# Kernel tuning notes

Measured on AMD Instinct MI355X. Metric: run time of the kernel, lower is better.

Reference implementation:

```python
import jax, jax.numpy as jnp
import numpy as np

N_RAYS = 16384
NS = 128
FD = 32
HID = 64
GS = 128
NEAR = 0.1
FAR = 100.0  # unused by the original forward body
EARLY_TERM = 1e-4


def mip360_contract(c):
    # inf-norm scene contraction (Mip-NeRF 360); safe denom avoids NaN grads in untaken branch
    norm = jnp.max(jnp.abs(c), axis=-1, keepdims=True)
    ns = jnp.maximum(norm, 1.0)
    return jnp.where(norm <= 1.0, c, (2.0 - 1.0 / ns) * c / ns) / 2.0


def grid_sample_trilinear(grid, coords):
    # torch.nn.functional.grid_sample 5D, mode='bilinear', padding='zeros', align_corners=False
    # grid: [D,H,W]; coords[...,0]=x->W, coords[...,1]=y->H, coords[...,2]=z->D, in [-1,1]
    D, H, W = grid.shape
    x = ((coords[..., 0] + 1.0) * W - 1.0) * 0.5
    y = ((coords[..., 1] + 1.0) * H - 1.0) * 0.5
    z = ((coords[..., 2] + 1.0) * D - 1.0) * 0.5
    x0 = jnp.floor(x); y0 = jnp.floor(y); z0 = jnp.floor(z)
    fx = x - x0; fy = y - y0; fz = z - z0
    x0 = x0.astype(jnp.int32); y0 = y0.astype(jnp.int32); z0 = z0.astype(jnp.int32)

    def corner(zi, yi, xi):
        valid = ((zi >= 0) & (zi < D) & (yi >= 0) & (yi < H) & (xi >= 0) & (xi < W))
        v = grid[jnp.clip(zi, 0, D - 1), jnp.clip(yi, 0, H - 1), jnp.clip(xi, 0, W - 1)]
        return v * valid.astype(grid.dtype)

    out = (corner(z0, y0, x0) * (1 - fz) * (1 - fy) * (1 - fx)
           + corner(z0, y0, x0 + 1) * (1 - fz) * (1 - fy) * fx
           + corner(z0, y0 + 1, x0) * (1 - fz) * fy * (1 - fx)
           + corner(z0, y0 + 1, x0 + 1) * (1 - fz) * fy * fx
           + corner(z0 + 1, y0, x0) * fz * (1 - fy) * (1 - fx)
           + corner(z0 + 1, y0, x0 + 1) * fz * (1 - fy) * fx
           + corner(z0 + 1, y0 + 1, x0) * fz * fy * (1 - fx)
           + corner(z0 + 1, y0 + 1, x0 + 1) * fz * fy * fx)
    return out


def setup_inputs() -> dict:
    key = jax.random.key(0)
    ks = jax.random.split(key, 9)
    rays_o = jax.random.normal(ks[0], (N_RAYS, 3), jnp.float32) * 0.1
    rd = jax.random.normal(ks[1], (N_RAYS, 3), jnp.float32)
    rays_d = rd / jnp.linalg.norm(rd, axis=-1, keepdims=True)
    grid = (jax.random.uniform(ks[2], (GS, GS, GS)) > 0.3).astype(jnp.float32)

    def lin(k, fin, fout):
        return jax.random.normal(k, (fin, fout), jnp.float32) * (1.0 / np.sqrt(fin))

    return {
        "rays_o": rays_o, "rays_d": rays_d, "grid": grid,
        "W1": lin(ks[3], 3, HID), "b1": jnp.zeros(HID, jnp.float32),
        "W2": lin(ks[4], HID, FD), "b2": jnp.zeros(FD, jnp.float32),
        "Ws": lin(ks[5], FD, 1), "bs": jnp.zeros(1, jnp.float32),
        "Wr1": lin(ks[6], FD + 3, HID), "br1": jnp.zeros(HID, jnp.float32),
        "Wr2": lin(ks[7], HID, 3), "br2": jnp.zeros(3, jnp.float32),
        "n_samples": NS,
    }


def reference(rays_o, rays_d, grid, W1, b1, W2, b2, Ws, bs, Wr1, br1, Wr2, br2, n_samples):
    n = rays_o.shape[0]
    half = n_samples // 2
    t_close = jnp.linspace(NEAR, NEAR + 1.0, half, dtype=jnp.float32)
    t_far = jnp.exp(jnp.arange(half, dtype=jnp.float32) * np.float32(np.log(1.0 + 1.0 / 256.0))) * (NEAR + 1.0)
    t_values = jnp.concatenate([t_close, t_far])
    distances = t_values[1:] - t_values[:-1]          # [S]
    t_values = t_values[:-1]                          # [S], S = n_samples - 1 (eval mode: no jitter)

    samples = rays_o[:, None, :] + rays_d[:, None, :] * t_values[None, :, None]   # [n,S,3]
    sc = mip360_contract(samples)
    occ = grid_sample_trilinear(grid, sc)             # [n,S]
    mask = occ > 0.0                                  # .bool() of sampled occupancy
    maskf = mask.astype(sc.dtype)

    # feature MLP; zero where unmasked (torch scatters into a zeros buffer)
    feat = jax.nn.relu(sc @ W1 + b1) @ W2 + b2        # [n,S,FD]
    feat = feat * maskf[..., None]
    sigma = jax.nn.softplus(feat @ Ws + bs)[..., 0] * maskf   # [n,S]

    alpha_log = -sigma * distances[None, :]
    trans = jnp.exp(jnp.cumsum(alpha_log, axis=1))
    trans = jnp.concatenate([jnp.ones((n, 1), sc.dtype), trans[:, :-1]], axis=1)
    alpha = 1.0 - jnp.exp(alpha_log)
    weights = trans * alpha                           # [n,S]

    mask2 = mask & (weights > EARLY_TERM)
    dirs = jnp.broadcast_to(rays_d[:, None, :], samples.shape)
    h = jax.nn.relu(jnp.concatenate([feat, dirs], axis=-1) @ Wr1 + br1)
    rgb = jax.nn.sigmoid(h @ Wr2 + br2) * weights[..., None]
    rgb = rgb * mask2[..., None].astype(sc.dtype)
    return rgb.sum(axis=1)                            # [n,3]
```

## Files before the change

### kernel.cpp

```cpp
#include <hip/hip_runtime.h>
#include <math.h>

#define HID 64
#define FD 32
#define ROWB 144

typedef __fp16 f16x8 __attribute__((ext_vector_type(8)));
typedef float  f32x4 __attribute__((ext_vector_type(4)));
typedef unsigned int u32x4 __attribute__((ext_vector_type(4)));
typedef unsigned int u32x2 __attribute__((ext_vector_type(2)));

__device__ __forceinline__ unsigned int pk2(float a, float b) {
    auto v = __builtin_amdgcn_cvt_pkrtz(a, b);
    return __builtin_bit_cast(unsigned int, v);
}
__device__ __forceinline__ f32x4 mfma16(f16x8 a, f16x8 b, f32x4 c) {
    return __builtin_amdgcn_mfma_f32_16x16x32_f16(a, b, c, 0, 0, 0);
}

__global__ void prep(const float* __restrict__ W2,  const float* __restrict__ Ws,
                     const float* __restrict__ bs,  const float* __restrict__ b2,
                     const float* __restrict__ Wr1, const float* __restrict__ Wr2,
                     unsigned char* __restrict__ wsb) {
    __shared__ float wv[64];
    const int t = threadIdx.x;
    if (t < 64) {
        float acc = 0.f;
        for (int k = 0; k < FD; ++k) acc = fmaf(W2[t*FD+k], Ws[k], acc);
        wv[t] = acc;
    }
    __syncthreads();
    if (t < 48) {
        float v = 0.f;
        if (t < 32) v = b2[t];
        else if (t == 32) {
            float c = bs[0];
            for (int k = 0; k < FD; ++k) c = fmaf(b2[k], Ws[k], c);
            v = c;
        }
        ((float*)(wsb + 16384))[t] = v;
    }
    const int f = t >> 6, lane = t & 63;
    const int c15 = lane & 15, g = lane >> 4;
    f16x8 o;
    #pragma unroll
    for (int j = 0; j < 8; ++j) {
        float v = 0.f;
        if (f < 6) {
            int mt = f >> 1, kc = f & 1, row = 16*mt + c15;
            int kg = 32*kc + 8*g + j;
            v = (row < 32) ? W2[kg*FD + row] : ((row == 32) ? wv[kg] : 0.f);
        } else if (f < 14) {
            int ff = f - 6, mt = ff >> 1, kc = ff & 1, row = 16*mt + c15;
            int kg = 32*kc + 8*g + j;
            v = (kg < FD+3) ? Wr1[kg*HID + row] : 0.f;
        } else {
            int kc = f - 14, row = c15;
            int kg = 32*kc + 8*g + j;
            v = (row < 3) ? Wr2[kg*3 + row] : 0.f;
        }
        o[j] = (__fp16)v;
    }
    *(f16x8*)(wsb + (f*64 + lane)*16) = o;
}

__device__ __forceinline__ float t_of(int i) {
    #pragma clang fp contract(off)
    if (i < 64) {
        if (i == 63) return 1.1f;
        return (float)(0.1 + (double)i * (1.0 / 63.0));
    }
    const float LOGC = 0.0038986404159402954f;
    float arg = (float)(i - 64) * LOGC;
    return (float)exp((double)arg) * 1.1f;
}

__device__ __forceinline__ bool gv(const float* __restrict__ g, int zi, int yi, int xi) {
    bool ok = ((unsigned)zi < 128u) & ((unsigned)yi < 128u) & ((unsigned)xi < 128u);
    int zc = min(max(zi, 0), 127);
    int yc = min(max(yi, 0), 127);
    int xc = min(max(xi, 0), 127);
    float v = g[(((zc << 7) + yc) << 7) + xc];
    return ok & (v > 0.5f);
}

__global__ __launch_bounds__(256) void nerf_render(
    const float* __restrict__ rays_o, const float* __restrict__ rays_d,
    const float* __restrict__ grid,
    const float* __restrict__ W1,  const float* __restrict__ b1,
    const float* __restrict__ br1, const float* __restrict__ br2,
    const unsigned char* __restrict__ wsb,
    float* __restrict__ out)
{
    __shared__ unsigned char lds[40960] __attribute__((aligned(16)));
    const int lane = threadIdx.x & 63;
    const int wid  = threadIdx.x >> 6;
    const int ray  = (blockIdx.x << 2) + wid;
    const int c15 = lane & 15, g = lane >> 4;

    unsigned char* ldsH = lds + wid*10240;
    float* ldsSig = (float*)(lds + wid*10240 + 9216);
    float* ldsRgb = (float*)(lds + wid*10240 + 9472);

    const f16x8* AF  = (const f16x8*)wsb;
    const float* b2e = (const float*)(wsb + 16384);

    const float ox = rays_o[ray*3+0], oy = rays_o[ray*3+1], oz = rays_o[ray*3+2];
    const float dx = rays_d[ray*3+0], dy = rays_d[ray*3+1], dz = rays_d[ray*3+2];

    f16x8 bd;
    #pragma unroll
    for (int j = 0; j < 8; ++j) bd[j] = (__fp16)0.f;
    if (g == 0) { bd[0] = (__fp16)dx; bd[1] = (__fp16)dy; bd[2] = (__fp16)dz; }

    float rr = 0.f, rg = 0.f, rb = 0.f;
    float carry = 0.f;

    #pragma unroll 1
    for (int chunk = 0; chunk < 2; ++chunk) {
        const int s  = (chunk << 6) + lane;
        const bool vs = (s < 127);
        const float tv = t_of(s);
        const float tn = t_of(s + 1);
        const float dist = tn - tv;

        float cx, cy, cz, fx, fy, fz;
        int x0, y0, z0;
        {
            #pragma clang fp contract(off)
            float px = ox + dx * tv;
            float py = oy + dy * tv;
            float pz = oz + dz * tv;
            float nrm = fmaxf(fabsf(px), fmaxf(fabsf(py), fabsf(pz)));
            if (nrm <= 1.0f) { cx = px; cy = py; cz = pz; }
            else {
                float t2 = 2.0f - 1.0f / nrm;
                cx = (t2 * px) / nrm; cy = (t2 * py) / nrm; cz = (t2 * pz) / nrm;
            }
            cx = cx * 0.5f; cy = cy * 0.5f; cz = cz * 0.5f;
            float gx = ((cx + 1.0f) * 128.0f - 1.0f) * 0.5f;
            float gy = ((cy + 1.0f) * 128.0f - 1.0f) * 0.5f;
            float gz = ((cz + 1.0f) * 128.0f - 1.0f) * 0.5f;
            float xf = floorf(gx), yf = floorf(gy), zf = floorf(gz);
            fx = gx - xf; fy = gy - yf; fz = gz - zf;
            x0 = (int)xf; y0 = (int)yf; z0 = (int)zf;
        }
        const bool fxp = fx > 0.f, fyp = fy > 0.f, fzp = fz > 0.f;
        bool m = gv(grid, z0,   y0,   x0)
             | (fxp             & gv(grid, z0,   y0,   x0+1))
             | (fyp             & gv(grid, z0,   y0+1, x0))
             | (fyp & fxp       & gv(grid, z0,   y0+1, x0+1))
             | (fzp             & gv(grid, z0+1, y0,   x0))
             | (fzp & fxp       & gv(grid, z0+1, y0,   x0+1))
             | (fzp & fyp       & gv(grid, z0+1, y0+1, x0))
             | (fzp & fyp & fxp & gv(grid, z0+1, y0+1, x0+1));
        m = m & vs;

        if (__ballot(m)) {
            {
                unsigned char* hw = ldsH + lane*ROWB;
                #pragma unroll
                for (int i = 0; i < 8; ++i) {
                    u32x4 wq;
                    #pragma unroll
                    for (int p = 0; p < 4; ++p) {
                        const int j0 = i*8 + p*2;
                        float h0 = b1[j0];
                        h0 = fmaf(cx, W1[j0], h0);
                        h0 = fmaf(cy, W1[HID + j0], h0);
                        h0 = fmaf(cz, W1[2*HID + j0], h0);
                        h0 = fmaxf(h0, 0.f);
                        float h1 = b1[j0+1];
                        h1 = fmaf(cx, W1[j0+1], h1);
                        h1 = fmaf(cy, W1[HID + j0+1], h1);
                        h1 = fmaf(cz, W1[2*HID + j0+1], h1);
                        h1 = fmaxf(h1, 0.f);
                        wq[p] = pk2(h0, h1);
                    }
                    *(u32x4*)(hw + i*16) = wq;
                }
            }
            f16x8 bh[4][2];
            #pragma unroll
            for (int nt = 0; nt < 4; ++nt)
                #pragma unroll
                for (int kc = 0; kc < 2; ++kc)
                    bh[nt][kc] = *(const f16x8*)(ldsH + (16*nt + c15)*ROWB + 64*kc + 16*g);

            float mfv[4];
            {
                int mi = __builtin_bit_cast(int, m ? 1.f : 0.f);
                #pragma unroll
                for (int nt = 0; nt < 4; ++nt)
                    mfv[nt] = __builtin_bit_cast(float,
                        __builtin_amdgcn_ds_bpermute((16*nt + c15) << 2, mi));
            }

            #pragma unroll
            for (int mt = 0; mt < 3; ++mt) {
                f16x8 a0 = AF[(mt*2+0)*64 + lane];
                f16x8 a1 = AF[(mt*2+1)*64 + lane];
                f32x4 acc[4];
                #pragma unroll
                for (int nt = 0; nt < 4; ++nt) { f32x4 z = {0.f,0.f,0.f,0.f}; acc[nt] = z; }
                #pragma unroll
                for (int nt = 0; nt < 4; ++nt) acc[nt] = mfma16(a0, bh[nt][0], acc[nt]);
                #pragma unroll
                for (int nt = 0; nt < 4; ++nt) acc[nt] = mfma16(a1, bh[nt][1], acc[nt]);
                f32x4 bb = *(const f32x4*)(b2e + 16*mt + 4*g);
                if (mt < 2) {
                    #pragma unroll
                    for (int nt = 0; nt < 4; ++nt) {
                        float v0 = (acc[nt][0] + bb[0]) * mfv[nt];
                        float v1 = (acc[nt][1] + bb[1]) * mfv[nt];
                        float v2 = (acc[nt][2] + bb[2]) * mfv[nt];
                        float v3 = (acc[nt][3] + bb[3]) * mfv[nt];
                        u32x2 w2; w2[0] = pk2(v0, v1); w2[1] = pk2(v2, v3);
                        *(u32x2*)(ldsH + (16*nt + c15)*ROWB + 32*mt + 8*g) = w2;
                    }
                } else if (g == 0) {
                    #pragma unroll
                    for (int nt = 0; nt < 4; ++nt)
                        ldsSig[16*nt + c15] = acc[nt][0] + bb[0];
                }
            }
            const float spre = ldsSig[lane];
            const float sp = fmaxf(spre, 0.f) + log1pf(expf(-fabsf(spre)));
            const float sigma = m ? sp : 0.f;
            const float al = -sigma * dist;

            float xs = al;
            #pragma unroll
            for (int d = 1; d < 64; d <<= 1) {
                float y = __shfl_up(xs, (unsigned)d, 64);
                if (lane >= d) xs += y;
            }
            const float total = __shfl(xs, 63, 64);
            const float trans = expf(carry + (xs - al));
            const float alpha = 1.0f - expf(al);
            const float w = trans * alpha;
            carry += total;

            const bool m2 = m & (w > 1e-4f);
            if (__ballot(m2)) {
                f16x8 bf[4];
                #pragma unroll
                for (int nt = 0; nt < 4; ++nt)
                    bf[nt] = *(const f16x8*)(ldsH + (16*nt + c15)*ROWB + 16*g);
                #pragma unroll
                for (int mt = 0; mt < 4; ++mt) {
                    f16x8 a0 = AF[(6 + mt*2 + 0)*64 + lane];
                    f16x8 a1 = AF[(6 + mt*2 + 1)*64 + lane];
                    f32x4 acc[4];
                    #pragma unroll
                    for (int nt = 0; nt < 4; ++nt) { f32x4 z = {0.f,0.f,0.f,0.f}; acc[nt] = z; }
                    #pragma unroll
                    for (int nt = 0; nt < 4; ++nt) acc[nt] = mfma16(a0, bf[nt], acc[nt]);
                    #pragma unroll
                    for (int nt = 0; nt < 4; ++nt) acc[nt] = mfma16(a1, bd, acc[nt]);
                    f32x4 bb = *(const f32x4*)(br1 + 16*mt + 4*g);
                    #pragma unroll
                    for (int nt = 0; nt < 4; ++nt) {
                        float v0 = fmaxf(acc[nt][0] + bb[0], 0.f);
                        float v1 = fmaxf(acc[nt][1] + bb[1], 0.f);
                        float v2 = fmaxf(acc[nt][2] + bb[2], 0.f);
                        float v3 = fmaxf(acc[nt][3] + bb[3], 0.f);
                        u32x2 w2; w2[0] = pk2(v0, v1); w2[1] = pk2(v2, v3);
                        *(u32x2*)(ldsH + (16*nt + c15)*ROWB + 32*mt + 8*g) = w2;
                    }
                }
                f16x8 a0 = AF[14*64 + lane];
                f16x8 a1 = AF[15*64 + lane];
                f32x4 accr[4];
                #pragma unroll
                for (int nt = 0; nt < 4; ++nt) {
                    f16x8 q0 = *(const f16x8*)(ldsH + (16*nt + c15)*ROWB + 16*g);
                    f16x8 q1 = *(const f16x8*)(ldsH + (16*nt + c15)*ROWB + 64 + 16*g);
                    f32x4 z = {0.f,0.f,0.f,0.f};
                    z = mfma16(a0, q0, z);
                    z = mfma16(a1, q1, z);
                    accr[nt] = z;
                }
                if (g == 0) {
                    const float c0 = br2[0], c1 = br2[1], c2 = br2[2];
                    #pragma unroll
                    for (int nt = 0; nt < 4; ++nt) {
                        float* rp = ldsRgb + (16*nt + c15)*3;
                        rp[0] = accr[nt][0] + c0;
                        rp[1] = accr[nt][1] + c1;
                        rp[2] = accr[nt][2] + c2;
                    }
                }
                const float* rp = ldsRgb + lane*3;
                const float l0 = rp[0], l1 = rp[1], l2 = rp[2];
                const float wm = m2 ? w : 0.f;
                rr = fmaf(1.f/(1.f + expf(-l0)), wm, rr);
                rg = fmaf(1.f/(1.f + expf(-l1)), wm, rg);
                rb = fmaf(1.f/(1.f + expf(-l2)), wm, rb);
            }
            if (chunk == 0 && expf(carry) <= 5e-5f) break;
        }
    }

    #pragma unroll
    for (int d = 32; d > 0; d >>= 1) {
        rr += __shfl_xor(rr, d, 64);
        rg += __shfl_xor(rg, d, 64);
        rb += __shfl_xor(rb, d, 64);
    }
    if (lane == 0) {
        out[ray*3+0] = rr;
        out[ray*3+1] = rg;
        out[ray*3+2] = rb;
    }
}

extern "C" void kernel_launch(void* const* d_in, const int* in_sizes, int n_in,
                              void* d_out, int out_size, void* d_ws, size_t ws_size,
                              hipStream_t stream) {
    const float* rays_o = (const float*)d_in[0];
    const float* rays_d = (const float*)d_in[1];
    const float* grid   = (const float*)d_in[2];
    const float* W1  = (const float*)d_in[3];
    const float* b1  = (const float*)d_in[4];
    const float* W2  = (const float*)d_in[5];
    const float* b2  = (const float*)d_in[6];
    const float* Ws  = (const float*)d_in[7];
    const float* bs  = (const float*)d_in[8];
    const float* Wr1 = (const float*)d_in[9];
    const float* br1 = (const float*)d_in[10];
    const float* Wr2 = (const float*)d_in[11];
    const float* br2 = (const float*)d_in[12];
    float* out = (float*)d_out;
    unsigned char* ws = (unsigned char*)d_ws;

    prep<<<dim3(1), dim3(1024), 0, stream>>>(W2, Ws, bs, b2, Wr1, Wr2, ws);
    nerf_render<<<dim3(16384/4), dim3(256), 0, stream>>>(
        rays_o, rays_d, grid, W1, b1, br1, br2, ws, out);
}
```

Baseline: 192.7 us.

## Move first MLP layer onto MFMA and use packed fp16 bias epilogues

The per-lane scalar FMA loop for the first layer (3→64 plus bias, ReLU) becomes an MFMA. Inputs are split into fp16 hi/lo parts, gathered across lanes with ds_bpermute, and the bias is folded in as an extra K column, with weights pre-packed in the prep kernel. Sample positions and interval widths come from a precomputed table instead of double-precision exp per sample. Bias-add and ReLU epilogues now use packed fp16 math, and the explicit feature mask multiply is dropped. This cuts VALU work and scalar weight loads, at the cost of fp16 rounding in bias adds and more prep-kernel work.

```diff
diff --git a/kernel.cpp b/kernel.cpp
--- a/kernel.cpp
+++ b/kernel.cpp
@@ -6,6 +6,7 @@
 #define ROWB 144
 
 typedef __fp16 f16x8 __attribute__((ext_vector_type(8)));
+typedef __fp16 f16x2v __attribute__((ext_vector_type(2)));
 typedef float  f32x4 __attribute__((ext_vector_type(4)));
 typedef unsigned int u32x4 __attribute__((ext_vector_type(4)));
 typedef unsigned int u32x2 __attribute__((ext_vector_type(2)));
@@ -14,13 +15,37 @@
     auto v = __builtin_amdgcn_cvt_pkrtz(a, b);
     return __builtin_bit_cast(unsigned int, v);
 }
+__device__ __forceinline__ unsigned int pkadd(unsigned int a, unsigned int b) {
+    f16x2v x = __builtin_bit_cast(f16x2v, a), y = __builtin_bit_cast(f16x2v, b);
+    f16x2v r = x + y;
+    return __builtin_bit_cast(unsigned int, r);
+}
+__device__ __forceinline__ unsigned int pkmax0(unsigned int a) {
+    f16x2v x = __builtin_bit_cast(f16x2v, a);
+    f16x2v z = {(__fp16)0.f, (__fp16)0.f};
+    f16x2v r = __builtin_elementwise_max(x, z);
+    return __builtin_bit_cast(unsigned int, r);
+}
 __device__ __forceinline__ f32x4 mfma16(f16x8 a, f16x8 b, f32x4 c) {
     return __builtin_amdgcn_mfma_f32_16x16x32_f16(a, b, c, 0, 0, 0);
 }
 
-__global__ void prep(const float* __restrict__ W2,  const float* __restrict__ Ws,
-                     const float* __restrict__ bs,  const float* __restrict__ b2,
-                     const float* __restrict__ Wr1, const float* __restrict__ Wr2,
+__device__ __forceinline__ float t_of(int i) {
+    #pragma clang fp contract(off)
+    if (i < 64) {
+        if (i == 63) return 1.1f;
+        return (float)(0.1 + (double)i * (1.0 / 63.0));
+    }
+    const float LOGC = 0.0038986404159402954f;
+    float arg = (float)(i - 64) * LOGC;
+    return (float)exp((double)arg) * 1.1f;
+}
+
+__global__ void prep(const float* __restrict__ W1, const float* __restrict__ b1,
+                     const float* __restrict__ W2, const float* __restrict__ b2,
+                     const float* __restrict__ Ws, const float* __restrict__ bs,
+                     const float* __restrict__ Wr1, const float* __restrict__ br1,
+                     const float* __restrict__ Wr2,
                      unsigned char* __restrict__ wsb) {
     __shared__ float wv[64];
     const int t = threadIdx.x;
@@ -30,6 +55,11 @@
         wv[t] = acc;
     }
     __syncthreads();
+    float* b2e = (float*)(wsb + 20480);
+    unsigned int* fpk  = (unsigned int*)(wsb + 20672);
+    unsigned int* r1pk = (unsigned int*)(wsb + 20736);
+    float* ttab = (float*)(wsb + 20864);
+    float* dtab = (float*)(wsb + 21376);
     if (t < 48) {
         float v = 0.f;
         if (t < 32) v = b2[t];
@@ -38,7 +68,18 @@
             for (int k = 0; k < FD; ++k) c = fmaf(b2[k], Ws[k], c);
             v = c;
         }
-        ((float*)(wsb + 16384))[t] = v;
+        b2e[t] = v;
+    }
+    if (t >= 64 && t < 192) { int s = t - 64; ttab[s] = t_of(s); dtab[s] = t_of(s+1) - t_of(s); }
+    if (t >= 192 && t < 208) {
+        int e = t - 192, mt = e >> 3, g = (e >> 1) & 3, p = e & 1;
+        int row = 16*mt + 4*g + 2*p;
+        fpk[e] = pk2(b2[row], b2[row+1]);
+    }
+    if (t >= 208 && t < 240) {
+        int e = t - 208, mt = e >> 3, g = (e >> 1) & 3, p = e & 1;
+        int row = 16*mt + 4*g + 2*p;
+        r1pk[e] = pk2(br1[row], br1[row+1]);
     }
     const int f = t >> 6, lane = t & 63;
     const int c15 = lane & 15, g = lane >> 4;
@@ -62,17 +103,19 @@
         o[j] = (__fp16)v;
     }
     *(f16x8*)(wsb + (f*64 + lane)*16) = o;
-}
-
-__device__ __forceinline__ float t_of(int i) {
-    #pragma clang fp contract(off)
-    if (i < 64) {
-        if (i == 63) return 1.1f;
-        return (float)(0.1 + (double)i * (1.0 / 63.0));
-    }
-    const float LOGC = 0.0038986404159402954f;
-    float arg = (float)(i - 64) * LOGC;
-    return (float)exp((double)arg) * 1.1f;
+    if (f < 4) {
+        f16x8 o2;
+        #pragma unroll
+        for (int j = 0; j < 8; ++j) {
+            int row = 16*f + c15, k = 8*g + j;
+            float v = 0.f;
+            if (k < 3)       v = W1[k*HID + row];
+            else if (k < 6)  v = W1[(k-3)*HID + row];
+            else if (k == 6) v = b1[row];
+            o2[j] = (__fp16)v;
+        }
+        *(f16x8*)(wsb + ((16+f)*64 + lane)*16) = o2;
+    }
 }
 
 __device__ __forceinline__ bool gv(const float* __restrict__ g, int zi, int yi, int xi) {
@@ -86,9 +129,7 @@
 
 __global__ __launch_bounds__(256) void nerf_render(
     const float* __restrict__ rays_o, const float* __restrict__ rays_d,
-    const float* __restrict__ grid,
-    const float* __restrict__ W1,  const float* __restrict__ b1,
-    const float* __restrict__ br1, const float* __restrict__ br2,
+    const float* __restrict__ grid,  const float* __restrict__ br2,
     const unsigned char* __restrict__ wsb,
     float* __restrict__ out)
 {
@@ -102,11 +143,23 @@
     float* ldsSig = (float*)(lds + wid*10240 + 9216);
     float* ldsRgb = (float*)(lds + wid*10240 + 9472);
 
-    const f16x8* AF  = (const f16x8*)wsb;
-    const float* b2e = (const float*)(wsb + 16384);
+    const f16x8* AF = (const f16x8*)wsb;
+    const float* b2e = (const float*)(wsb + 20480);
+    const unsigned int* fpk  = (const unsigned int*)(wsb + 20672);
+    const unsigned int* r1pk = (const unsigned int*)(wsb + 20736);
+    const float* ttab = (const float*)(wsb + 20864);
+    const float* dtab = (const float*)(wsb + 21376);
 
     const float ox = rays_o[ray*3+0], oy = rays_o[ray*3+1], oz = rays_o[ray*3+2];
     const float dx = rays_d[ray*3+0], dy = rays_d[ray*3+1], dz = rays_d[ray*3+2];
+
+    const float b2e32 = b2e[32];
+    unsigned int fpkv[2][2], r1pkv[4][2];
+    #pragma unroll
+    for (int mt = 0; mt < 2; ++mt) { fpkv[mt][0] = fpk[mt*8+g*2]; fpkv[mt][1] = fpk[mt*8+g*2+1]; }
+    #pragma unroll
+    for (int mt = 0; mt < 4; ++mt) { r1pkv[mt][0] = r1pk[mt*8+g*2]; r1pkv[mt][1] = r1pk[mt*8+g*2+1]; }
+    const unsigned int p3c = pk2(1.f, 0.f);
 
     f16x8 bd;
     #pragma unroll
@@ -120,9 +173,8 @@
     for (int chunk = 0; chunk < 2; ++chunk) {
         const int s  = (chunk << 6) + lane;
         const bool vs = (s < 127);
-        const float tv = t_of(s);
-        const float tn = t_of(s + 1);
-        const float dist = tn - tv;
+        const float tv = ttab[s];
+        const float dist = dtab[s];
 
         float cx, cy, cz, fx, fy, fz;
         int x0, y0, z0;
@@ -157,27 +209,33 @@
         m = m & vs;
 
         if (__ballot(m)) {
-            {
-                unsigned char* hw = ldsH + lane*ROWB;
-                #pragma unroll
-                for (int i = 0; i < 8; ++i) {
-                    u32x4 wq;
-                    #pragma unroll
-                    for (int p = 0; p < 4; ++p) {
-                        const int j0 = i*8 + p*2;
-                        float h0 = b1[j0];
-                        h0 = fmaf(cx, W1[j0], h0);
-                        h0 = fmaf(cy, W1[HID + j0], h0);
-                        h0 = fmaf(cz, W1[2*HID + j0], h0);
-                        h0 = fmaxf(h0, 0.f);
-                        float h1 = b1[j0+1];
-                        h1 = fmaf(cx, W1[j0+1], h1);
-                        h1 = fmaf(cy, W1[HID + j0+1], h1);
-                        h1 = fmaf(cz, W1[2*HID + j0+1], h1);
-                        h1 = fmaxf(h1, 0.f);
-                        wq[p] = pk2(h0, h1);
-                    }
-                    *(u32x4*)(hw + i*16) = wq;
+            float xh = (float)(__fp16)cx, yh = (float)(__fp16)cy, zh = (float)(__fp16)cz;
+            unsigned int q0 = pk2(xh, yh);
+            unsigned int q1 = pk2(zh, cx - xh);
+            unsigned int q2 = pk2(cy - yh, cz - zh);
+
+            f16x8 bl1[4];
+            #pragma unroll
+            for (int nt = 0; nt < 4; ++nt) {
+                int ad = (16*nt + c15) << 2;
+                u32x4 bw;
+                bw[0] = (unsigned int)__builtin_amdgcn_ds_bpermute(ad, (int)q0);
+                bw[1] = (unsigned int)__builtin_amdgcn_ds_bpermute(ad, (int)q1);
+                bw[2] = (unsigned int)__builtin_amdgcn_ds_bpermute(ad, (int)q2);
+                bw[3] = p3c;
+                bl1[nt] = __builtin_bit_cast(f16x8, bw);
+            }
+            #pragma unroll
+            for (int mt = 0; mt < 4; ++mt) {
+                f16x8 a = AF[(16+mt)*64 + lane];
+                #pragma unroll
+                for (int nt = 0; nt < 4; ++nt) {
+                    f32x4 z = {0.f,0.f,0.f,0.f};
+                    z = mfma16(a, bl1[nt], z);
+                    u32x2 ww;
+                    ww[0] = pkmax0(pk2(z[0], z[1]));
+                    ww[1] = pkmax0(pk2(z[2], z[3]));
+                    *(u32x2*)(ldsH + (16*nt + c15)*ROWB + 32*mt + 8*g) = ww;
                 }
             }
             f16x8 bh[4][2];
@@ -186,15 +244,6 @@
                 #pragma unroll
                 for (int kc = 0; kc < 2; ++kc)
                     bh[nt][kc] = *(const f16x8*)(ldsH + (16*nt + c15)*ROWB + 64*kc + 16*g);
-
-            float mfv[4];
-            {
-                int mi = __builtin_bit_cast(int, m ? 1.f : 0.f);
-                #pragma unroll
-                for (int nt = 0; nt < 4; ++nt)
-                    mfv[nt] = __builtin_bit_cast(float,
-                        __builtin_amdgcn_ds_bpermute((16*nt + c15) << 2, mi));
-            }
 
             #pragma unroll
             for (int mt = 0; mt < 3; ++mt) {
@@ -207,21 +256,18 @@
                 for (int nt = 0; nt < 4; ++nt) acc[nt] = mfma16(a0, bh[nt][0], acc[nt]);
                 #pragma unroll
                 for (int nt = 0; nt < 4; ++nt) acc[nt] = mfma16(a1, bh[nt][1], acc[nt]);
-                f32x4 bb = *(const f32x4*)(b2e + 16*mt + 4*g);
                 if (mt < 2) {
                     #pragma unroll
                     for (int nt = 0; nt < 4; ++nt) {
-                        float v0 = (acc[nt][0] + bb[0]) * mfv[nt];
-                        float v1 = (acc[nt][1] + bb[1]) * mfv[nt];
-                        float v2 = (acc[nt][2] + bb[2]) * mfv[nt];
-                        float v3 = (acc[nt][3] + bb[3]) * mfv[nt];
-                        u32x2 w2; w2[0] = pk2(v0, v1); w2[1] = pk2(v2, v3);
-                        *(u32x2*)(ldsH + (16*nt + c15)*ROWB + 32*mt + 8*g) = w2;
+                        u32x2 ww;
+                        ww[0] = pkadd(pk2(acc[nt][0], acc[nt][1]), fpkv[mt][0]);
+                        ww[1] = pkadd(pk2(acc[nt][2], acc[nt][3]), fpkv[mt][1]);
+                        *(u32x2*)(ldsH + (16*nt + c15)*ROWB + 32*mt + 8*g) = ww;
                     }
                 } else if (g == 0) {
                     #pragma unroll
                     for (int nt = 0; nt < 4; ++nt)
-                        ldsSig[16*nt + c15] = acc[nt][0] + bb[0];
+                        ldsSig[16*nt + c15] = acc[nt][0] + b2e32;
                 }
             }
             const float spre = ldsSig[lane];
@@ -258,15 +304,12 @@
                     for (int nt = 0; nt < 4; ++nt) acc[nt] = mfma16(a0, bf[nt], acc[nt]);
                     #pragma unroll
                     for (int nt = 0; nt < 4; ++nt) acc[nt] = mfma16(a1, bd, acc[nt]);
-                    f32x4 bb = *(const f32x4*)(br1 + 16*mt + 4*g);
                     #pragma unroll
                     for (int nt = 0; nt < 4; ++nt) {
-                        float v0 = fmaxf(acc[nt][0] + bb[0], 0.f);
-                        float v1 = fmaxf(acc[nt][1] + bb[1], 0.f);
-                        float v2 = fmaxf(acc[nt][2] + bb[2], 0.f);
-                        float v3 = fmaxf(acc[nt][3] + bb[3], 0.f);
-                        u32x2 w2; w2[0] = pk2(v0, v1); w2[1] = pk2(v2, v3);
-                        *(u32x2*)(ldsH + (16*nt + c15)*ROWB + 32*mt + 8*g) = w2;
+                        u32x2 ww;
+                        ww[0] = pkmax0(pkadd(pk2(acc[nt][0], acc[nt][1]), r1pkv[mt][0]));
+                        ww[1] = pkmax0(pkadd(pk2(acc[nt][2], acc[nt][3]), r1pkv[mt][1]));
+                        *(u32x2*)(ldsH + (16*nt + c15)*ROWB + 32*mt + 8*g) = ww;
                     }
                 }
                 f16x8 a0 = AF[14*64 + lane];
@@ -274,11 +317,11 @@
                 f32x4 accr[4];
                 #pragma unroll
                 for (int nt = 0; nt < 4; ++nt) {
-                    f16x8 q0 = *(const f16x8*)(ldsH + (16*nt + c15)*ROWB + 16*g);
-                    f16x8 q1 = *(const f16x8*)(ldsH + (16*nt + c15)*ROWB + 64 + 16*g);
+                    f16x8 q0c = *(const f16x8*)(ldsH + (16*nt + c15)*ROWB + 16*g);
+                    f16x8 q1c = *(const f16x8*)(ldsH + (16*nt + c15)*ROWB + 64 + 16*g);
                     f32x4 z = {0.f,0.f,0.f,0.f};
-                    z = mfma16(a0, q0, z);
-                    z = mfma16(a1, q1, z);
+                    z = mfma16(a0, q0c, z);
+                    z = mfma16(a1, q1c, z);
                     accr[nt] = z;
                 }
                 if (g == 0) {
@@ -334,7 +377,7 @@
     float* out = (float*)d_out;
     unsigned char* ws = (unsigned char*)d_ws;
 
-    prep<<<dim3(1), dim3(1024), 0, stream>>>(W2, Ws, bs, b2, Wr1, Wr2, ws);
+    prep<<<dim3(1), dim3(1024), 0, stream>>>(W1, b1, W2, b2, Ws, bs, Wr1, br1, Wr2, ws);
     nerf_render<<<dim3(16384/4), dim3(256), 0, stream>>>(
-        rays_o, rays_d, grid, W1, b1, br1, br2, ws, out);
-}
+        rays_o, rays_d, grid, br2, ws, out);
+}
```

Result: faster. 175.8 us (-8.7%).
